# Performance work log

Hardware: AMD Instinct MI355X
Metric: run time of the kernel (lower is better)

## Reference

```python
import jax, jax.numpy as jnp
import numpy as np

NUM_HEADS = 12


def setup_inputs() -> dict:
    key = jax.random.key(0)
    k1, k2, k3 = jax.random.split(key, 3)
    B, N, D = 8, 1024, 768
    x = jax.random.normal(k1, (B, N, D), dtype=jnp.float32)
    Wqkv = jax.random.normal(k2, (D, 3 * D), dtype=jnp.float32) * (D ** -0.5)
    Wproj = jax.random.normal(k3, (D, D), dtype=jnp.float32) * (D ** -0.5)
    bproj = jnp.zeros((D,), dtype=jnp.float32)
    return {"x": x, "Wqkv": Wqkv, "Wproj": Wproj, "bproj": bproj}


def reference(x, Wqkv, Wproj, bproj):
    B, N, D = x.shape
    H = NUM_HEADS
    d = D // H
    scale = d ** -0.5
    qkv = x @ Wqkv  # [B, N, 3D]; qkv_bias=False
    # 'b n (qkv h d) -> qkv b h n d'
    qkv = qkv.reshape(B, N, 3, H, d)
    q = jnp.transpose(qkv[:, :, 0], (0, 2, 1, 3))  # [B, H, N, d]
    k = jnp.transpose(qkv[:, :, 1], (0, 2, 1, 3))
    v = jnp.transpose(qkv[:, :, 2], (0, 2, 1, 3))
    attn = jnp.einsum('bhnd,bhmd->bhnm', q, k) * scale  # [B, H, N, N]
    attn = jax.nn.softmax(attn, axis=-1)
    out = jnp.einsum('bhnm,bhmd->bhnd', attn, v)  # [B, H, N, d]
    out = jnp.transpose(out, (0, 2, 1, 3)).reshape(B, N, D)  # 'b h n d -> b n (h d)'
    return out @ Wproj + bproj
```

## Files before the change

### kernel.cpp

```cpp
#include <hip/hip_runtime.h>
#include <math.h>
#include <stdint.h>

namespace {

constexpr int Nseq = 1024;
constexpr int Dm = 768;
constexpr int threeD = 2304;
constexpr int Mrows = 8192;
constexpr int Hh = 12;
constexpr float kScaleLog2 = 0.18033688011112042f;

using bf16x8 = __attribute__((ext_vector_type(8))) short;
using f32x4 = __attribute__((ext_vector_type(4))) float;
using f32x16 = __attribute__((ext_vector_type(16))) float;
using us4 = __attribute__((ext_vector_type(4))) unsigned short;

__device__ __forceinline__ unsigned short f2bf(float f) {
  union { float f; uint32_t u; } v;
  v.f = f;
  uint32_t r = v.u + 0x7fffu + ((v.u >> 16) & 1u);
  return (unsigned short)(r >> 16);
}

__device__ __forceinline__ float fexp2(float x) {
#if __has_builtin(__builtin_amdgcn_exp2f)
  return __builtin_amdgcn_exp2f(x);
#else
  float r;
  asm("v_exp_f32 %0, %1\n\ts_nop 0" : "=v"(r) : "v"(x));
  return r;
#endif
}

__device__ __forceinline__ uint32_t cvtpk_bf16(float lo, float hi) {
  uint32_t r;
  asm("v_cvt_pk_bf16_f32 %0, %1, %2" : "=v"(r) : "v"(lo), "v"(hi));
  return r;
}

__device__ __forceinline__ void gload_lds16(const void* g, void* l) {
  __builtin_amdgcn_global_load_lds(
      (const __attribute__((address_space(1))) unsigned int*)(uintptr_t)g,
      (__attribute__((address_space(3))) unsigned int*)(uintptr_t)l, 16, 0, 0);
}

__global__ __launch_bounds__(256) void prep_all(
    const float* __restrict__ x, const float* __restrict__ Wqkv,
    const float* __restrict__ Wproj, unsigned short* __restrict__ xb,
    unsigned short* __restrict__ wqkvt, unsigned short* __restrict__ wprojt) {
  __shared__ unsigned short tile[32][33];
  const int bid = blockIdx.x;
  if (bid < 6144) {
    const int i = bid * 256 + threadIdx.x;
    float4 v = ((const float4*)x)[i];
    us4 u = {f2bf(v.x), f2bf(v.y), f2bf(v.z), f2bf(v.w)};
    ((us4*)xb)[i] = u;
    return;
  }
  const float* W;
  unsigned short* Wt;
  int N, t;
  if (bid < 6144 + 1728) {
    W = Wqkv;
    Wt = wqkvt;
    N = threeD;
    t = bid - 6144;
  } else {
    W = Wproj;
    Wt = wprojt;
    N = Dm;
    t = bid - 6144 - 1728;
  }
  const int nx = N / 32;
  const int n0 = (t % nx) * 32, k0 = (t / nx) * 32;
  const int tx = threadIdx.x & 31, ty = threadIdx.x >> 5;
#pragma unroll
  for (int i = 0; i < 32; i += 8)
    tile[ty + i][tx] = f2bf(W[(size_t)(k0 + ty + i) * N + n0 + tx]);
  __syncthreads();
#pragma unroll
  for (int i = 0; i < 32; i += 8)
    Wt[(size_t)(n0 + ty + i) * 768 + k0 + tx] = tile[tx][ty + i];
}

__global__ __launch_bounds__(256) void gemm_qkv64(
    const unsigned short* __restrict__ A, const unsigned short* __restrict__ Bt,
    unsigned short* __restrict__ C0, unsigned short* __restrict__ C1) {
  constexpr int K = Dm;
  constexpr int NTK = K / 64;
  constexpr int NCOLS = 18;
  __shared__ unsigned short As[2][128 * 64];
  __shared__ unsigned short Bs[2][128 * 64];
  const int tid = threadIdx.x;
  const int wid = tid >> 6;
  const int lane = tid & 63;
  const int l15 = lane & 15, lg = lane >> 4;
  const int p = blockIdx.x;
  const int cpx = gridDim.x >> 3;
  const int l = (p & 7) * cpx + (p >> 3);
  const int row0 = (l / NCOLS) * 128, col0 = (l % NCOLS) * 128;
  const int wr = (wid >> 1) * 64, wc = (wid & 1) * 64;

  auto stage = [&](int kt, int bufi) {
    unsigned short* as = As[bufi];
    unsigned short* bs = Bs[bufi];
#pragma unroll
    for (int it = 0; it < 4; ++it) {
      const int s = it * 256 + tid;
      const int r = s >> 3, c = s & 7;
      const int g = c ^ (r & 7);
      gload_lds16(&A[(size_t)(row0 + r) * K + kt * 64 + g * 8],
                  &as[(s & ~63) * 8]);
    }
#pragma unroll
    for (int it = 0; it < 4; ++it) {
      const int s = it * 256 + tid;
      const int r = s >> 3, c = s & 7;
      const int g = c ^ (r & 7);
      gload_lds16(&Bt[(size_t)(col0 + r) * K + kt * 64 + g * 8],
                  &bs[(s & ~63) * 8]);
    }
  };

  f32x4 acc[4][4] = {};
  stage(0, 0);
  for (int g = 0; g < NTK; ++g) {
    const int cur = g & 1;
    if (g + 1 < NTK) {
      stage(g + 1, cur ^ 1);
      asm volatile("s_waitcnt vmcnt(8)" ::: "memory");
    } else {
      asm volatile("s_waitcnt vmcnt(0)" ::: "memory");
    }
    __builtin_amdgcn_s_barrier();
#pragma unroll
    for (int ks = 0; ks < 2; ++ks) {
      bf16x8 av[4], bv[4];
#pragma unroll
      for (int m = 0; m < 4; ++m) {
        const int ar = wr + m * 16 + l15;
        const int sc = (ks * 4 + lg) ^ (ar & 7);
        av[m] = *(const bf16x8*)&As[cur][(ar * 8 + sc) * 8];
      }
#pragma unroll
      for (int n = 0; n < 4; ++n) {
        const int br = wc + n * 16 + l15;
        const int sc = (ks * 4 + lg) ^ (br & 7);
        bv[n] = *(const bf16x8*)&Bs[cur][(br * 8 + sc) * 8];
      }
      __builtin_amdgcn_s_setprio(1);
#pragma unroll
      for (int m = 0; m < 4; ++m)
#pragma unroll
        for (int n = 0; n < 4; ++n)
          acc[m][n] = __builtin_amdgcn_mfma_f32_16x16x32_bf16(av[m], bv[n],
                                                              acc[m][n], 0, 0, 0);
      __builtin_amdgcn_s_setprio(0);
    }
    asm volatile("s_waitcnt lgkmcnt(0)" ::: "memory");
    __builtin_amdgcn_sched_barrier(0);
    __builtin_amdgcn_s_barrier();
  }
  if (col0 < 1536) {
#pragma unroll
    for (int m = 0; m < 4; ++m)
#pragma unroll
      for (int n = 0; n < 4; ++n) {
        const int col = col0 + wc + n * 16 + l15;
        const float qs = (col < 768) ? kScaleLog2 : 1.f;
#pragma unroll
        for (int rr = 0; rr < 4; ++rr)
          C0[(size_t)(row0 + wr + m * 16 + lg * 4 + rr) * 1536 + col] =
              f2bf(acc[m][n][rr] * qs);
      }
  } else {
#pragma unroll
    for (int m = 0; m < 4; ++m)
#pragma unroll
      for (int n = 0; n < 4; ++n) {
        const int c = col0 + wc + n * 16 + l15 - 1536;
        const int row = row0 + wr + m * 16 + lg * 4;
        const int bb = row >> 10, n0 = row & 1023;
        us4 pk = {f2bf(acc[m][n][0]), f2bf(acc[m][n][1]), f2bf(acc[m][n][2]),
                  f2bf(acc[m][n][3])};
        *(us4*)&C1[((size_t)bb * 768 + c) * 1024 + n0] = pk;
      }
  }
}

__global__ __launch_bounds__(256) void gemm_proj64(
    const unsigned short* __restrict__ A, const unsigned short* __restrict__ Bt,
    float* __restrict__ C0, const float* __restrict__ bias) {
  constexpr int K = Dm;
  constexpr int NTK = K / 64;
  constexpr int NCOLS = 6;
  __shared__ unsigned short As[2][64 * 64];
  __shared__ unsigned short Bs[2][128 * 64];
  const int tid = threadIdx.x;
  const int wid = tid >> 6;
  const int lane = tid & 63;
  const int l15 = lane & 15, lg = lane >> 4;
  const int p = blockIdx.x;
  const int cpx = gridDim.x >> 3;
  const int l = (p & 7) * cpx + (p >> 3);
  const int row0 = (l / NCOLS) * 64, col0 = (l % NCOLS) * 128;
  const int wr = (wid >> 1) * 32, wc = (wid & 1) * 64;

  auto stage = [&](int kt, int bufi) {
    unsigned short* as = As[bufi];
    unsigned short* bs = Bs[bufi];
#pragma unroll
    for (int it = 0; it < 2; ++it) {
      const int s = it * 256 + tid;
      const int r = s >> 3, c = s & 7;
      const int g = c ^ (r & 7);
      gload_lds16(&A[(size_t)(row0 + r) * K + kt * 64 + g * 8],
                  &as[(s & ~63) * 8]);
    }
#pragma unroll
    for (int it = 0; it < 4; ++it) {
      const int s = it * 256 + tid;
      const int r = s >> 3, c = s & 7;
      const int g = c ^ (r & 7);
      gload_lds16(&Bt[(size_t)(col0 + r) * K + kt * 64 + g * 8],
                  &bs[(s & ~63) * 8]);
    }
  };

  f32x4 acc[2][4] = {};
  stage(0, 0);
  for (int g = 0; g < NTK; ++g) {
    const int cur = g & 1;
    if (g + 1 < NTK) {
      stage(g + 1, cur ^ 1);
      asm volatile("s_waitcnt vmcnt(6)" ::: "memory");
    } else {
      asm volatile("s_waitcnt vmcnt(0)" ::: "memory");
    }
    __builtin_amdgcn_s_barrier();
#pragma unroll
    for (int ks = 0; ks < 2; ++ks) {
      bf16x8 av[2], bv[4];
#pragma unroll
      for (int m = 0; m < 2; ++m) {
        const int ar = wr + m * 16 + l15;
        const int sc = (ks * 4 + lg) ^ (ar & 7);
        av[m] = *(const bf16x8*)&As[cur][(ar * 8 + sc) * 8];
      }
#pragma unroll
      for (int n = 0; n < 4; ++n) {
        const int br = wc + n * 16 + l15;
        const int sc = (ks * 4 + lg) ^ (br & 7);
        bv[n] = *(const bf16x8*)&Bs[cur][(br * 8 + sc) * 8];
      }
      __builtin_amdgcn_s_setprio(1);
#pragma unroll
      for (int m = 0; m < 2; ++m)
#pragma unroll
        for (int n = 0; n < 4; ++n)
          acc[m][n] = __builtin_amdgcn_mfma_f32_16x16x32_bf16(av[m], bv[n],
                                                              acc[m][n], 0, 0, 0);
      __builtin_amdgcn_s_setprio(0);
    }
    asm volatile("s_waitcnt lgkmcnt(0)" ::: "memory");
    __builtin_amdgcn_sched_barrier(0);
    __builtin_amdgcn_s_barrier();
  }
#pragma unroll
  for (int m = 0; m < 2; ++m)
#pragma unroll
    for (int n = 0; n < 4; ++n) {
      const int col = col0 + wc + n * 16 + l15;
#pragma unroll
      for (int rr = 0; rr < 4; ++rr)
        C0[(size_t)(row0 + wr + m * 16 + lg * 4 + rr) * Dm + col] =
            acc[m][n][rr] + bias[col];
    }
}

__global__ __launch_bounds__(512, 4) void attn_mfma(
    const unsigned short* __restrict__ qkb, const unsigned short* __restrict__ vtb,
    unsigned short* __restrict__ outb) {
  constexpr int NT = Nseq / 64;
  __shared__ unsigned short Ks[2][64 * 64];
  __shared__ unsigned short Vs[2][64 * 64];
  const int tid = threadIdx.x;
  const int wid = tid >> 6, lane = tid & 63;
  const int l31 = lane & 31, hi = lane >> 5;
  const int p = blockIdx.x;
  const int l = (p & 7) * 48 + (p >> 3);
  const int qt2 = l & 3;
  const int hb = l >> 2;
  const int h = hb % Hh, b = hb / Hh;
  const size_t rb = (size_t)b * Nseq;
  const int hoff = h * 64;
  const size_t vbase = ((size_t)b * 768 + hoff) * 1024;

  const int qrow = qt2 * 256 + wid * 32 + l31;
  bf16x8 Qf[4];
#pragma unroll
  for (int ks = 0; ks < 4; ++ks)
    Qf[ks] = *(const bf16x8*)&qkb[(rb + qrow) * 1536 + hoff + ks * 16 + hi * 8];

  const int strow = tid >> 3;
  const int scol = ((tid & 7) ^ (strow & 7)) * 8;
  const int ldsoff = (wid * 64) * 8;

  auto stage = [&](int kt, int bufi) {
    gload_lds16(&qkb[(rb + kt * 64 + strow) * 1536 + 768 + hoff + scol],
                &Ks[bufi][ldsoff]);
    gload_lds16(&vtb[vbase + (size_t)strow * 1024 + kt * 64 + scol],
                &Vs[bufi][ldsoff]);
  };

  float l_run = 0.f;
  f32x16 o0 = {}, o1 = {};

  stage(0, 0);
  for (int kt = 0; kt < NT; ++kt) {
    const int bufi = kt & 1;
    if (kt + 1 < NT) {
      stage(kt + 1, bufi ^ 1);
      asm volatile("s_waitcnt vmcnt(2)" ::: "memory");
    } else {
      asm volatile("s_waitcnt vmcnt(0)" ::: "memory");
    }
    __builtin_amdgcn_s_barrier();
    const unsigned short* ksb = Ks[bufi];
    const unsigned short* vsb = Vs[bufi];
    f32x16 s0 = {}, s1 = {};
    __builtin_amdgcn_s_setprio(1);
#pragma unroll
    for (int ks = 0; ks < 4; ++ks) {
      const int c = 2 * ks + hi;
      {
        const int tr = l31;
        bf16x8 kf = *(const bf16x8*)&ksb[tr * 64 + ((c ^ (tr & 7)) * 8)];
        s0 = __builtin_amdgcn_mfma_f32_32x32x16_bf16(kf, Qf[ks], s0, 0, 0, 0);
      }
      {
        const int tr = l31 + 32;
        bf16x8 kf = *(const bf16x8*)&ksb[tr * 64 + ((c ^ (tr & 7)) * 8)];
        s1 = __builtin_amdgcn_mfma_f32_32x32x16_bf16(kf, Qf[ks], s1, 0, 0, 0);
      }
    }
    __builtin_amdgcn_s_setprio(0);
#pragma unroll
    for (int i = 0; i < 16; ++i) {
      s0[i] = fexp2(s0[i]);
      s1[i] = fexp2(s1[i]);
    }
    float a[8];
#pragma unroll
    for (int i = 0; i < 8; ++i)
      a[i] = (s0[i] + s0[i + 8]) + (s1[i] + s1[i + 8]);
#pragma unroll
    for (int st = 4; st >= 1; st >>= 1)
#pragma unroll
      for (int i = 0; i < st; ++i) a[i] += a[i + st];
    l_run += a[0];
    bf16x8 Pf[4];
#pragma unroll
    for (int ks = 0; ks < 4; ++ks) {
      const f32x16 sv = (ks >> 1) ? s1 : s0;
      const int e0 = 8 * (ks & 1);
      uint32_t pe01 = cvtpk_bf16(sv[e0 + 0], sv[e0 + 1]);
      uint32_t pe23 = cvtpk_bf16(sv[e0 + 2], sv[e0 + 3]);
      uint32_t po01 = cvtpk_bf16(sv[e0 + 4], sv[e0 + 5]);
      uint32_t po23 = cvtpk_bf16(sv[e0 + 6], sv[e0 + 7]);
      asm("v_permlane32_swap_b32 %0, %1" : "+v"(pe01), "+v"(po01));
      asm("v_permlane32_swap_b32 %0, %1" : "+v"(pe23), "+v"(po23));
      union {
        uint32_t w[4];
        bf16x8 v;
      } u;
      u.w[0] = pe01;
      u.w[1] = pe23;
      u.w[2] = po01;
      u.w[3] = po23;
      Pf[ks] = u.v;
    }
    __builtin_amdgcn_s_setprio(1);
#pragma unroll
    for (int ks = 0; ks < 4; ++ks) {
      const int c = 2 * ks + hi;
      {
        const int tr = l31;
        bf16x8 vf = *(const bf16x8*)&vsb[tr * 64 + ((c ^ (tr & 7)) * 8)];
        o0 = __builtin_amdgcn_mfma_f32_32x32x16_bf16(vf, Pf[ks], o0, 0, 0, 0);
      }
      {
        const int tr = l31 + 32;
        bf16x8 vf = *(const bf16x8*)&vsb[tr * 64 + ((c ^ (tr & 7)) * 8)];
        o1 = __builtin_amdgcn_mfma_f32_32x32x16_bf16(vf, Pf[ks], o1, 0, 0, 0);
      }
    }
    __builtin_amdgcn_s_setprio(0);
    asm volatile("s_waitcnt lgkmcnt(0)" ::: "memory");
    __builtin_amdgcn_sched_barrier(0);
    __builtin_amdgcn_s_barrier();
  }
  const float lsum = l_run + __shfl_xor(l_run, 32);
  const float linv = 1.f / lsum;
  const size_t obase = (size_t)(rb + qrow) * Dm + hoff;
#pragma unroll
  for (int g = 0; g < 4; ++g) {
    us4 a4 = {f2bf(o0[g * 4 + 0] * linv), f2bf(o0[g * 4 + 1] * linv),
              f2bf(o0[g * 4 + 2] * linv), f2bf(o0[g * 4 + 3] * linv)};
    *(us4*)&outb[obase + g * 8 + hi * 4] = a4;
    us4 b4 = {f2bf(o1[g * 4 + 0] * linv), f2bf(o1[g * 4 + 1] * linv),
              f2bf(o1[g * 4 + 2] * linv), f2bf(o1[g * 4 + 3] * linv)};
    *(us4*)&outb[obase + 32 + g * 8 + hi * 4] = b4;
  }
}

}

extern "C" void kernel_launch(void* const* d_in, const int* in_sizes, int n_in,
                              void* d_out, int out_size, void* d_ws,
                              size_t ws_size, hipStream_t stream) {
  (void)in_sizes;
  (void)n_in;
  (void)out_size;
  (void)ws_size;
  const float* x = (const float*)d_in[0];
  const float* Wqkv = (const float*)d_in[1];
  const float* Wproj = (const float*)d_in[2];
  const float* bproj = (const float*)d_in[3];
  float* out = (float*)d_out;

  char* w = (char*)d_ws;
  unsigned short* xb = (unsigned short*)w;
  w += (size_t)Mrows * Dm * 2;
  unsigned short* wqkvt = (unsigned short*)w;
  w += (size_t)threeD * Dm * 2;
  unsigned short* wprojt = (unsigned short*)w;
  w += (size_t)Dm * Dm * 2;
  unsigned short* qkb = (unsigned short*)w;
  w += (size_t)Mrows * 1536 * 2;
  unsigned short* vtb = (unsigned short*)w;
  w += (size_t)96 * 64 * 1024 * 2;
  unsigned short* attnb = (unsigned short*)w;

  prep_all<<<dim3(6144 + 1728 + 576), 256, 0, stream>>>(x, Wqkv, Wproj, xb,
                                                        wqkvt, wprojt);
  gemm_qkv64<<<dim3(1152), 256, 0, stream>>>(xb, wqkvt, qkb, vtb);
  attn_mfma<<<dim3(384), 512, 0, stream>>>(qkb, vtb, attnb);
  gemm_proj64<<<dim3(768), 256, 0, stream>>>(attnb, wprojt, out, bproj);
}
```

Baseline: 108.6 us.

## Process two 32-row query tiles per wave in attention, halving block threads

```diff
diff --git a/kernel.cpp b/kernel.cpp
--- a/kernel.cpp
+++ b/kernel.cpp
@@ -279,7 +279,7 @@
     }
 }
 
-__global__ __launch_bounds__(512, 4) void attn_mfma(
+__global__ __launch_bounds__(256, 2) void attn_mfma(
     const unsigned short* __restrict__ qkb, const unsigned short* __restrict__ vtb,
     unsigned short* __restrict__ outb) {
   constexpr int NT = Nseq / 64;
@@ -297,121 +297,172 @@
   const int hoff = h * 64;
   const size_t vbase = ((size_t)b * 768 + hoff) * 1024;
 
-  const int qrow = qt2 * 256 + wid * 32 + l31;
-  bf16x8 Qf[4];
-#pragma unroll
-  for (int ks = 0; ks < 4; ++ks)
-    Qf[ks] = *(const bf16x8*)&qkb[(rb + qrow) * 1536 + hoff + ks * 16 + hi * 8];
-
-  const int strow = tid >> 3;
-  const int scol = ((tid & 7) ^ (strow & 7)) * 8;
-  const int ldsoff = (wid * 64) * 8;
+  const int qrowA = qt2 * 256 + wid * 64 + l31;
+  const int qrowB = qrowA + 32;
+  bf16x8 QfA[4], QfB[4];
+#pragma unroll
+  for (int ks = 0; ks < 4; ++ks) {
+    QfA[ks] = *(const bf16x8*)&qkb[(rb + qrowA) * 1536 + hoff + ks * 16 + hi * 8];
+    QfB[ks] = *(const bf16x8*)&qkb[(rb + qrowB) * 1536 + hoff + ks * 16 + hi * 8];
+  }
+
+  int strow[2], scol[2];
+#pragma unroll
+  for (int it = 0; it < 2; ++it) {
+    const int ci = it * 256 + tid;
+    const int tr = ci >> 3, cc = ci & 7;
+    strow[it] = tr;
+    scol[it] = (cc ^ (tr & 7)) * 8;
+  }
 
   auto stage = [&](int kt, int bufi) {
-    gload_lds16(&qkb[(rb + kt * 64 + strow) * 1536 + 768 + hoff + scol],
-                &Ks[bufi][ldsoff]);
-    gload_lds16(&vtb[vbase + (size_t)strow * 1024 + kt * 64 + scol],
-                &Vs[bufi][ldsoff]);
+#pragma unroll
+    for (int it = 0; it < 2; ++it) {
+      const int ldsoff = (it * 256 + wid * 64) * 8;
+      gload_lds16(&qkb[(rb + kt * 64 + strow[it]) * 1536 + 768 + hoff + scol[it]],
+                  &Ks[bufi][ldsoff]);
+      gload_lds16(&vtb[vbase + (size_t)strow[it] * 1024 + kt * 64 + scol[it]],
+                  &Vs[bufi][ldsoff]);
+    }
   };
 
-  float l_run = 0.f;
-  f32x16 o0 = {}, o1 = {};
+  float l_runA = 0.f, l_runB = 0.f;
+  f32x16 oA0 = {}, oA1 = {}, oB0 = {}, oB1 = {};
 
   stage(0, 0);
   for (int kt = 0; kt < NT; ++kt) {
     const int bufi = kt & 1;
     if (kt + 1 < NT) {
       stage(kt + 1, bufi ^ 1);
-      asm volatile("s_waitcnt vmcnt(2)" ::: "memory");
+      asm volatile("s_waitcnt vmcnt(4)" ::: "memory");
     } else {
       asm volatile("s_waitcnt vmcnt(0)" ::: "memory");
     }
     __builtin_amdgcn_s_barrier();
     const unsigned short* ksb = Ks[bufi];
     const unsigned short* vsb = Vs[bufi];
-    f32x16 s0 = {}, s1 = {};
+    f32x16 sA0 = {}, sA1 = {}, sB0 = {}, sB1 = {};
     __builtin_amdgcn_s_setprio(1);
 #pragma unroll
     for (int ks = 0; ks < 4; ++ks) {
       const int c = 2 * ks + hi;
+      const int trl = l31, trh = l31 + 32;
+      bf16x8 kfl = *(const bf16x8*)&ksb[trl * 64 + ((c ^ (trl & 7)) * 8)];
+      bf16x8 kfh = *(const bf16x8*)&ksb[trh * 64 + ((c ^ (trh & 7)) * 8)];
+      sA0 = __builtin_amdgcn_mfma_f32_32x32x16_bf16(kfl, QfA[ks], sA0, 0, 0, 0);
+      sA1 = __builtin_amdgcn_mfma_f32_32x32x16_bf16(kfh, QfA[ks], sA1, 0, 0, 0);
+      sB0 = __builtin_amdgcn_mfma_f32_32x32x16_bf16(kfl, QfB[ks], sB0, 0, 0, 0);
+      sB1 = __builtin_amdgcn_mfma_f32_32x32x16_bf16(kfh, QfB[ks], sB1, 0, 0, 0);
+    }
+    __builtin_amdgcn_s_setprio(0);
+#pragma unroll
+    for (int i = 0; i < 16; ++i) {
+      sA0[i] = fexp2(sA0[i]);
+      sA1[i] = fexp2(sA1[i]);
+      sB0[i] = fexp2(sB0[i]);
+      sB1[i] = fexp2(sB1[i]);
+    }
+    {
+      float a[8];
+#pragma unroll
+      for (int i = 0; i < 8; ++i)
+        a[i] = (sA0[i] + sA0[i + 8]) + (sA1[i] + sA1[i + 8]);
+#pragma unroll
+      for (int st = 4; st >= 1; st >>= 1)
+#pragma unroll
+        for (int i = 0; i < st; ++i) a[i] += a[i + st];
+      l_runA += a[0];
+    }
+    {
+      float a[8];
+#pragma unroll
+      for (int i = 0; i < 8; ++i)
+        a[i] = (sB0[i] + sB0[i + 8]) + (sB1[i] + sB1[i + 8]);
+#pragma unroll
+      for (int st = 4; st >= 1; st >>= 1)
+#pragma unroll
+        for (int i = 0; i < st; ++i) a[i] += a[i + st];
+      l_runB += a[0];
+    }
+    bf16x8 PfA[4], PfB[4];
+#pragma unroll
+    for (int ks = 0; ks < 4; ++ks) {
       {
-        const int tr = l31;
-        bf16x8 kf = *(const bf16x8*)&ksb[tr * 64 + ((c ^ (tr & 7)) * 8)];
-        s0 = __builtin_amdgcn_mfma_f32_32x32x16_bf16(kf, Qf[ks], s0, 0, 0, 0);
+        const f32x16 sv = (ks >> 1) ? sA1 : sA0;
+        const int e0 = 8 * (ks & 1);
+        uint32_t pe01 = cvtpk_bf16(sv[e0 + 0], sv[e0 + 1]);
+        uint32_t pe23 = cvtpk_bf16(sv[e0 + 2], sv[e0 + 3]);
+        uint32_t po01 = cvtpk_bf16(sv[e0 + 4], sv[e0 + 5]);
+        uint32_t po23 = cvtpk_bf16(sv[e0 + 6], sv[e0 + 7]);
+        asm("v_permlane32_swap_b32 %0, %1" : "+v"(pe01), "+v"(po01));
+        asm("v_permlane32_swap_b32 %0, %1" : "+v"(pe23), "+v"(po23));
+        union {
+          uint32_t w[4];
+          bf16x8 v;
+        } u;
+        u.w[0] = pe01;
+        u.w[1] = pe23;
+        u.w[2] = po01;
+        u.w[3] = po23;
+        PfA[ks] = u.v;
       }
       {
-        const int tr = l31 + 32;
-        bf16x8 kf = *(const bf16x8*)&ksb[tr * 64 + ((c ^ (tr & 7)) * 8)];
-        s1 = __builtin_amdgcn_mfma_f32_32x32x16_bf16(kf, Qf[ks], s1, 0, 0, 0);
-      }
-    }
-    __builtin_amdgcn_s_setprio(0);
-#pragma unroll
-    for (int i = 0; i < 16; ++i) {
-      s0[i] = fexp2(s0[i]);
-      s1[i] = fexp2(s1[i]);
-    }
-    float a[8];
-#pragma unroll
-    for (int i = 0; i < 8; ++i)
-      a[i] = (s0[i] + s0[i + 8]) + (s1[i] + s1[i + 8]);
-#pragma unroll
-    for (int st = 4; st >= 1; st >>= 1)
-#pragma unroll
-      for (int i = 0; i < st; ++i) a[i] += a[i + st];
-    l_run += a[0];
-    bf16x8 Pf[4];
-#pragma unroll
-    for (int ks = 0; ks < 4; ++ks) {
-      const f32x16 sv = (ks >> 1) ? s1 : s0;
-      const int e0 = 8 * (ks & 1);
-      uint32_t pe01 = cvtpk_bf16(sv[e0 + 0], sv[e0 + 1]);
-      uint32_t pe23 = cvtpk_bf16(sv[e0 + 2], sv[e0 + 3]);
-      uint32_t po01 = cvtpk_bf16(sv[e0 + 4], sv[e0 + 5]);
-      uint32_t po23 = cvtpk_bf16(sv[e0 + 6], sv[e0 + 7]);
-      asm("v_permlane32_swap_b32 %0, %1" : "+v"(pe01), "+v"(po01));
-      asm("v_permlane32_swap_b32 %0, %1" : "+v"(pe23), "+v"(po23));
-      union {
-        uint32_t w[4];
-        bf16x8 v;
-      } u;
-      u.w[0] = pe01;
-      u.w[1] = pe23;
-      u.w[2] = po01;
-      u.w[3] = po23;
-      Pf[ks] = u.v;
+        const f32x16 sv = (ks >> 1) ? sB1 : sB0;
+        const int e0 = 8 * (ks & 1);
+        uint32_t pe01 = cvtpk_bf16(sv[e0 + 0], sv[e0 + 1]);
+        uint32_t pe23 = cvtpk_bf16(sv[e0 + 2], sv[e0 + 3]);
+        uint32_t po01 = cvtpk_bf16(sv[e0 + 4], sv[e0 + 5]);
+        uint32_t po23 = cvtpk_bf16(sv[e0 + 6], sv[e0 + 7]);
+        asm("v_permlane32_swap_b32 %0, %1" : "+v"(pe01), "+v"(po01));
+        asm("v_permlane32_swap_b32 %0, %1" : "+v"(pe23), "+v"(po23));
+        union {
+          uint32_t w[4];
+          bf16x8 v;
+        } u;
+        u.w[0] = pe01;
+        u.w[1] = pe23;
+        u.w[2] = po01;
+        u.w[3] = po23;
+        PfB[ks] = u.v;
+      }
     }
     __builtin_amdgcn_s_setprio(1);
 #pragma unroll
     for (int ks = 0; ks < 4; ++ks) {
       const int c = 2 * ks + hi;
-      {
-        const int tr = l31;
-        bf16x8 vf = *(const bf16x8*)&vsb[tr * 64 + ((c ^ (tr & 7)) * 8)];
-        o0 = __builtin_amdgcn_mfma_f32_32x32x16_bf16(vf, Pf[ks], o0, 0, 0, 0);
-      }
-      {
-        const int tr = l31 + 32;
-        bf16x8 vf = *(const bf16x8*)&vsb[tr * 64 + ((c ^ (tr & 7)) * 8)];
-        o1 = __builtin_amdgcn_mfma_f32_32x32x16_bf16(vf, Pf[ks], o1, 0, 0, 0);
-      }
+      const int trl = l31, trh = l31 + 32;
+      bf16x8 vfl = *(const bf16x8*)&vsb[trl * 64 + ((c ^ (trl & 7)) * 8)];
+      bf16x8 vfh = *(const bf16x8*)&vsb[trh * 64 + ((c ^ (trh & 7)) * 8)];
+      oA0 = __builtin_amdgcn_mfma_f32_32x32x16_bf16(vfl, PfA[ks], oA0, 0, 0, 0);
+      oA1 = __builtin_amdgcn_mfma_f32_32x32x16_bf16(vfh, PfA[ks], oA1, 0, 0, 0);
+      oB0 = __builtin_amdgcn_mfma_f32_32x32x16_bf16(vfl, PfB[ks], oB0, 0, 0, 0);
+      oB1 = __builtin_amdgcn_mfma_f32_32x32x16_bf16(vfh, PfB[ks], oB1, 0, 0, 0);
     }
     __builtin_amdgcn_s_setprio(0);
     asm volatile("s_waitcnt lgkmcnt(0)" ::: "memory");
     __builtin_amdgcn_sched_barrier(0);
     __builtin_amdgcn_s_barrier();
   }
-  const float lsum = l_run + __shfl_xor(l_run, 32);
-  const float linv = 1.f / lsum;
-  const size_t obase = (size_t)(rb + qrow) * Dm + hoff;
+  const float lsumA = l_runA + __shfl_xor(l_runA, 32);
+  const float lsumB = l_runB + __shfl_xor(l_runB, 32);
+  const float linvA = 1.f / lsumA;
+  const float linvB = 1.f / lsumB;
+  const size_t obaseA = (size_t)(rb + qrowA) * Dm + hoff;
+  const size_t obaseB = (size_t)(rb + qrowB) * Dm + hoff;
 #pragma unroll
   for (int g = 0; g < 4; ++g) {
-    us4 a4 = {f2bf(o0[g * 4 + 0] * linv), f2bf(o0[g * 4 + 1] * linv),
-              f2bf(o0[g * 4 + 2] * linv), f2bf(o0[g * 4 + 3] * linv)};
-    *(us4*)&outb[obase + g * 8 + hi * 4] = a4;
-    us4 b4 = {f2bf(o1[g * 4 + 0] * linv), f2bf(o1[g * 4 + 1] * linv),
-              f2bf(o1[g * 4 + 2] * linv), f2bf(o1[g * 4 + 3] * linv)};
-    *(us4*)&outb[obase + 32 + g * 8 + hi * 4] = b4;
+    us4 a4 = {f2bf(oA0[g * 4 + 0] * linvA), f2bf(oA0[g * 4 + 1] * linvA),
+              f2bf(oA0[g * 4 + 2] * linvA), f2bf(oA0[g * 4 + 3] * linvA)};
+    *(us4*)&outb[obaseA + g * 8 + hi * 4] = a4;
+    us4 a5 = {f2bf(oA1[g * 4 + 0] * linvA), f2bf(oA1[g * 4 + 1] * linvA),
+              f2bf(oA1[g * 4 + 2] * linvA), f2bf(oA1[g * 4 + 3] * linvA)};
+    *(us4*)&outb[obaseA + 32 + g * 8 + hi * 4] = a5;
+    us4 b4 = {f2bf(oB0[g * 4 + 0] * linvB), f2bf(oB0[g * 4 + 1] * linvB),
+              f2bf(oB0[g * 4 + 2] * linvB), f2bf(oB0[g * 4 + 3] * linvB)};
+    *(us4*)&outb[obaseB + g * 8 + hi * 4] = b4;
+    us4 b5 = {f2bf(oB1[g * 4 + 0] * linvB), f2bf(oB1[g * 4 + 1] * linvB),
+              f2bf(oB1[g * 4 + 2] * linvB), f2bf(oB1[g * 4 + 3] * linvB)};
+    *(us4*)&outb[obaseB + 32 + g * 8 + hi * 4] = b5;
   }
 }
 
@@ -446,6 +497,6 @@
   prep_all<<<dim3(6144 + 1728 + 576), 256, 0, stream>>>(x, Wqkv, Wproj, xb,
                                                         wqkvt, wprojt);
   gemm_qkv64<<<dim3(1152), 256, 0, stream>>>(xb, wqkvt, qkb, vtb);
-  attn_mfma<<<dim3(384), 512, 0, stream>>>(qkb, vtb, attnb);
+  attn_mfma<<<dim3(384), 256, 0, stream>>>(qkb, vtb, attnb);
   gemm_proj64<<<dim3(768), 256, 0, stream>>>(attnb, wprojt, out, bproj);
 }
```

Result: no change. 109.4 us (+0.8%).
